# Kernel tuning notes

Measured on AMD Instinct MI355X. Metric: run time of the kernel, lower is better.

## Reference

```python
import jax, jax.numpy as jnp
import numpy as np


def _log_g(x):
    # log of g(x) = x + 0.5 for x >= 0, sigmoid(x) for x < 0 (minGRU paper, log-space)
    return jnp.where(x >= 0, jnp.log(jax.nn.relu(x) + 0.5), -jax.nn.softplus(-x))


def setup_inputs() -> dict:
    key = jax.random.key(0)
    k1, k2, k3 = jax.random.split(key, 3)
    B, L, D, H = 4, 8192, 512, 1024
    x = jax.random.normal(k1, (B, L, D), dtype=jnp.float32)
    # 1x1 conv in-projection to [hidden | gate], scaled for sane activation magnitudes
    W_in = jax.random.normal(k2, (2 * H, D), dtype=jnp.float32) * 0.05
    b_in = jnp.zeros((2 * H,), dtype=jnp.float32)
    # 1x1 conv out-projection back to model dim
    W_out = jax.random.normal(k3, (D, H), dtype=jnp.float32) * 0.05
    b_out = jnp.zeros((D,), dtype=jnp.float32)
    return {"x": x, "W_in": W_in, "b_in": b_in, "W_out": W_out, "b_out": b_out}


def reference(x, W_in, b_in, W_out, b_out):
    # x: [B, L, D]. tokenMixer transposes to [B, D, L] for MinGRU (1x1 convs),
    # which is equivalent to pointwise matmuls over the channel dim here.
    hg = jnp.einsum('bld,ed->ble', x, W_in) + b_in          # [B, L, 2H]
    H = hg.shape[-1] // 2
    hidden, gate = hg[..., :H], hg[..., H:]

    # minGRU log-space parallel scan (Heinsen associative scan):
    # h_t = (1 - z_t) * h_{t-1} + z_t * g(hidden_t), z_t = sigmoid(gate_t)
    log_coeffs = -jax.nn.softplus(gate)      # log(1 - z_t)
    log_z = -jax.nn.softplus(-gate)          # log(z_t)
    log_tilde_h = _log_g(hidden)             # log(g(hidden_t))

    a_star = jnp.cumsum(log_coeffs, axis=1)                              # [B, L, H]
    log_h = a_star + jax.lax.cumlogsumexp(log_z + log_tilde_h - a_star, axis=1)
    h = jnp.exp(log_h)                                                   # [B, L, H]

    out = jnp.einsum('blh,dh->bld', h, W_out) + b_out                    # [B, L, D]
    return out
```

## Files before the change

kernel.cpp:

```cpp
#include <hip/hip_runtime.h>
#include <hip/hip_bf16.h>
#include <cstdint>
#include <cstddef>

#define B_ 4
#define L_ 8192
#define D_ 512
#define H_ 1024
#define NC_ 256
#define LC_ (L_ / NC_)

typedef float  f32x4 __attribute__((ext_vector_type(4)));
typedef short  s16x8 __attribute__((ext_vector_type(8)));
typedef __bf16 b16x8 __attribute__((ext_vector_type(8)));

template <typename T, typename U>
__device__ inline auto mfma_sel(T a, T b, f32x4 c, U, int)
    -> decltype(__builtin_amdgcn_mfma_f32_16x16x32_bf16(a, b, c, 0, 0, 0)) {
  return __builtin_amdgcn_mfma_f32_16x16x32_bf16(a, b, c, 0, 0, 0);
}
template <typename T, typename U>
__device__ inline f32x4 mfma_sel(T a, T b, f32x4 c, U, long) {
  return __builtin_amdgcn_mfma_f32_16x16x32_bf16(
      __builtin_bit_cast(U, a), __builtin_bit_cast(U, b), c, 0, 0, 0);
}
__device__ inline f32x4 mfma_bf16_16x16x32(s16x8 a, s16x8 b, f32x4 c) {
  return mfma_sel(a, b, c, b16x8{}, 0);
}

__device__ inline ushort f2bf(float f) {
  uint32_t u = __builtin_bit_cast(uint32_t, f);
  uint32_t r = (u + 0x7fffu + ((u >> 16) & 1u)) >> 16;
  return (ushort)r;
}
__device__ inline float bf2f(ushort u) {
  return __builtin_bit_cast(float, (uint32_t)u << 16);
}

__device__ inline float softplus_f(float x) {
  return fmaxf(x, 0.f) + __logf(1.f + __expf(-fabsf(x)));
}
__device__ inline float logaddexp_f(float a, float b) {
  float m = fmaxf(a, b);
  return m + __logf(1.f + __expf(-fabsf(a - b)));
}
__device__ inline void transform_f(float hd, float g, float& lc, float& v) {
  float sp = softplus_f(g);
  lc = -sp;
  float lz = g - sp;
  float lth = (hd >= 0.f) ? __logf(hd + 0.5f) : (hd - softplus_f(hd));
  v = lz + lth;
}

__global__ void cast_kernel(const float* __restrict__ in, ushort* __restrict__ out, int n4) {
  int i = blockIdx.x * blockDim.x + threadIdx.x;
  if (i >= n4) return;
  float4 f = reinterpret_cast<const float4*>(in)[i];
  ushort4 o;
  o.x = f2bf(f.x); o.y = f2bf(f.y); o.z = f2bf(f.z); o.w = f2bf(f.w);
  reinterpret_cast<ushort4*>(out)[i] = o;
}

__global__ void cast2_kernel(const float* __restrict__ in0, ushort* __restrict__ out0, int n4_0,
                             const float* __restrict__ in1, ushort* __restrict__ out1, int n4_1) {
  int i = blockIdx.x * blockDim.x + threadIdx.x;
  const float* in; ushort* out;
  if (i < n4_0) { in = in0; out = out0; }
  else { i -= n4_0; if (i >= n4_1) return; in = in1; out = out1; }
  float4 f = reinterpret_cast<const float4*>(in)[i];
  ushort4 o;
  o.x = f2bf(f.x); o.y = f2bf(f.y); o.z = f2bf(f.z); o.w = f2bf(f.w);
  reinterpret_cast<ushort4*>(out)[i] = o;
}

#define GLDS(srcp, dstp)                                                            \
  __builtin_amdgcn_global_load_lds(                                                 \
      (const __attribute__((address_space(1))) void*)(srcp),                        \
      (__attribute__((address_space(3))) void*)(dstp), 16, 0, 0)

#define BAR()                               \
  do {                                      \
    asm volatile("" ::: "memory");          \
    __builtin_amdgcn_s_barrier();           \
    asm volatile("" ::: "memory");          \
  } while (0)

template <int MODE>
__global__ __launch_bounds__(512, 2)
void gemm_bt(const ushort* __restrict__ A, const ushort* __restrict__ Bm,
             const float* __restrict__ bias, void* __restrict__ Cv,
             int M, int N, int K) {
  __shared__ ushort As[2][256 * 64];
  __shared__ ushort Bs[2][256 * 64];
  const int tid  = threadIdx.x;
  const int wave = tid >> 6;
  const int lane = tid & 63;
  const int l15  = lane & 15;
  const int quad = lane >> 4;

  int id = blockIdx.y * gridDim.x + blockIdx.x;
  const int nwg = gridDim.x * gridDim.y;
  id = (id & 7) * (nwg >> 3) + (id >> 3);
  const int bxi = id % gridDim.x;
  const int byi = id / gridDim.x;

  const long bm = (long)byi * 256;
  const long bn = (long)bxi * 256;
  const int  wm = (wave >> 2) * 128;

  f32x4 acc[8][4];
#pragma unroll
  for (int i = 0; i < 8; ++i)
#pragma unroll
    for (int j = 0; j < 4; ++j) acc[i][j] = (f32x4){0.f, 0.f, 0.f, 0.f};

  const int rl  = lane >> 3;
  const int cb  = (lane & 7) ^ rl;
  const int srow = wave * 32 + rl;
  const ushort* gA0 = A + (bm + srow) * (long)K + cb * 8;
  const ushort* gB0;
  if (MODE == 1) {
    const long n0 = bn >> 1;
    const long grow = (srow < 128) ? (n0 + srow) : (1024 + n0 + (srow - 128));
    gB0 = Bm + grow * (long)K + cb * 8;
  } else {
    gB0 = Bm + (bn + srow) * (long)K + cb * 8;
  }
  int ldst[4];
#pragma unroll
  for (int i = 0; i < 4; ++i) ldst[i] = (wave * 32 + 8 * i) * 64;

  const int sq0 = ((0 * 4 + quad) ^ (l15 & 7)) * 8;
  const int sq1 = ((1 * 4 + quad) ^ (l15 & 7)) * 8;
  int arow[8], brow[4];
#pragma unroll
  for (int i = 0; i < 8; ++i) arow[i] = (wm + i * 16 + l15) * 64;
  if (MODE == 1) {
    const int wn0 = (wave & 3) * 32;
#pragma unroll
    for (int j = 0; j < 4; ++j) {
      const int trow = (j < 2) ? (wn0 + j * 16) : (128 + wn0 + (j - 2) * 16);
      brow[j] = (trow + l15) * 64;
    }
  } else {
    const int wn = (wave & 3) * 64;
#pragma unroll
    for (int j = 0; j < 4; ++j) brow[j] = (wn + j * 16 + l15) * 64;
  }

  const int nkt = K >> 6;

#pragma unroll
  for (int i = 0; i < 4; ++i) GLDS(gA0 + 8L * i * K, &As[0][ldst[i]]);
#pragma unroll
  for (int i = 0; i < 4; ++i) GLDS(gB0 + 8L * i * K, &Bs[0][ldst[i]]);
  asm volatile("s_waitcnt vmcnt(0)" ::: "memory");
  BAR();

  for (int t = 0; t < nkt; ++t) {
    const int buf  = t & 1;
    const int nbuf = buf ^ 1;
    const bool pf  = (t + 1) < nkt;
    const ushort* Ac = As[buf];
    const ushort* Bc = Bs[buf];
    const long koff = (long)(t + 1) * 64;
    s16x8 bf[4], af[4];

#pragma unroll
    for (int j = 0; j < 4; ++j)
      bf[j] = *reinterpret_cast<const s16x8*>(&Bc[brow[j] + sq0]);
#pragma unroll
    for (int i = 0; i < 4; ++i)
      af[i] = *reinterpret_cast<const s16x8*>(&Ac[arow[i] + sq0]);
    if (pf) {
#pragma unroll
      for (int i = 0; i < 4; ++i) GLDS(gA0 + 8L * i * K + koff, &As[nbuf][ldst[i]]);
    }
    BAR();
    __builtin_amdgcn_s_setprio(1);
#pragma unroll
    for (int i = 0; i < 4; ++i)
#pragma unroll
      for (int j = 0; j < 4; ++j)
        acc[i][j] = mfma_bf16_16x16x32(af[i], bf[j], acc[i][j]);
    __builtin_amdgcn_s_setprio(0);
    BAR();

#pragma unroll
    for (int i = 0; i < 4; ++i)
      af[i] = *reinterpret_cast<const s16x8*>(&Ac[arow[4 + i] + sq0]);
    if (pf) {
#pragma unroll
      for (int i = 0; i < 4; ++i) GLDS(gB0 + 8L * i * K + koff, &Bs[nbuf][ldst[i]]);
    }
    BAR();
    __builtin_amdgcn_s_setprio(1);
#pragma unroll
    for (int i = 0; i < 4; ++i)
#pragma unroll
      for (int j = 0; j < 4; ++j)
        acc[4 + i][j] = mfma_bf16_16x16x32(af[i], bf[j], acc[4 + i][j]);
    __builtin_amdgcn_s_setprio(0);
    BAR();

#pragma unroll
    for (int j = 0; j < 4; ++j)
      bf[j] = *reinterpret_cast<const s16x8*>(&Bc[brow[j] + sq1]);
#pragma unroll
    for (int i = 0; i < 4; ++i)
      af[i] = *reinterpret_cast<const s16x8*>(&Ac[arow[i] + sq1]);
    BAR();
    __builtin_amdgcn_s_setprio(1);
#pragma unroll
    for (int i = 0; i < 4; ++i)
#pragma unroll
      for (int j = 0; j < 4; ++j)
        acc[i][j] = mfma_bf16_16x16x32(af[i], bf[j], acc[i][j]);
    __builtin_amdgcn_s_setprio(0);
    BAR();

#pragma unroll
    for (int i = 0; i < 4; ++i)
      af[i] = *reinterpret_cast<const s16x8*>(&Ac[arow[4 + i] + sq1]);
    BAR();
    __builtin_amdgcn_s_setprio(1);
#pragma unroll
    for (int i = 0; i < 4; ++i)
#pragma unroll
      for (int j = 0; j < 4; ++j)
        acc[4 + i][j] = mfma_bf16_16x16x32(af[i], bf[j], acc[4 + i][j]);
    __builtin_amdgcn_s_setprio(0);
    if (pf) asm volatile("s_waitcnt vmcnt(0)" ::: "memory");
    BAR();
  }

  if (MODE == 1) {
    const long n0  = bn >> 1;
    const int  wn0 = (wave & 3) * 32;
#pragma unroll
    for (int mi = 0; mi < 8; ++mi) {
      const long mrow = bm + wm + mi * 16 + quad * 4;
#pragma unroll
      for (int j = 0; j < 2; ++j) {
        const long ch = n0 + wn0 + j * 16 + l15;
        const float bh = bias[ch];
        const float bg = bias[(long)(N >> 1) + ch];
        ushort* lp = (ushort*)Cv + mrow * (long)N + ch;
#pragma unroll
        for (int r = 0; r < 4; ++r) {
          float hd = acc[mi][j][r] + bh;
          float g  = acc[mi][j + 2][r] + bg;
          float lc, v; transform_f(hd, g, lc, v);
          lp[(long)r * N] = f2bf(lc);
          lp[(long)r * N + (N >> 1)] = f2bf(v);
        }
      }
    }
  } else {
    const int wn = (wave & 3) * 64;
#pragma unroll
    for (int mi = 0; mi < 8; ++mi) {
      const long mrow = bm + wm + mi * 16 + quad * 4;
#pragma unroll
      for (int ni = 0; ni < 4; ++ni) {
        const long ncol = bn + wn + ni * 16 + l15;
        const float bv = bias[ncol];
        float* cp = (float*)Cv + mrow * (long)N + ncol;
#pragma unroll
        for (int r = 0; r < 4; ++r) cp[(long)r * N] = acc[mi][ni][r] + bv;
      }
    }
  }
}

__global__ void scan_phase1(const ushort* __restrict__ hg,
                            float* __restrict__ Ac, float* __restrict__ Bc) {
  int gid = blockIdx.x * blockDim.x + threadIdx.x;
  int hq = gid & (H_ / 4 - 1);
  int c  = (gid >> 8) & (NC_ - 1);
  int b  = gid >> 16;
  const ushort* p = hg + ((size_t)(b * L_ + c * LC_) * (2 * H_)) + hq * 4;
  float As[4] = {0.f, 0.f, 0.f, 0.f};
  float Bv[4] = {-INFINITY, -INFINITY, -INFINITY, -INFINITY};
#pragma unroll 4
  for (int l = 0; l < LC_; ++l) {
    ushort4 lc4 = *reinterpret_cast<const ushort4*>(p);
    ushort4 v4  = *reinterpret_cast<const ushort4*>(p + H_);
    float lcv[4] = {bf2f(lc4.x), bf2f(lc4.y), bf2f(lc4.z), bf2f(lc4.w)};
    float vv[4]  = {bf2f(v4.x),  bf2f(v4.y),  bf2f(v4.z),  bf2f(v4.w)};
#pragma unroll
    for (int j = 0; j < 4; ++j) {
      As[j] += lcv[j];
      Bv[j] = logaddexp_f(Bv[j] + lcv[j], vv[j]);
    }
    p += 2 * H_;
  }
  size_t o = (size_t)(b * NC_ + c) * H_ + hq * 4;
  *reinterpret_cast<float4*>(&Ac[o]) = make_float4(As[0], As[1], As[2], As[3]);
  *reinterpret_cast<float4*>(&Bc[o]) = make_float4(Bv[0], Bv[1], Bv[2], Bv[3]);
}

__global__ void scan_phase2(const float* __restrict__ Ac, const float* __restrict__ Bc,
                            float* __restrict__ carry) {
  int gid = blockIdx.x * blockDim.x + threadIdx.x;
  int h = gid & (H_ - 1);
  int b = gid >> 10;
  float P = -INFINITY;
  for (int c = 0; c < NC_; ++c) {
    size_t o = (size_t)(b * NC_ + c) * H_ + h;
    carry[o] = P;
    P = logaddexp_f(P + Ac[o], Bc[o]);
  }
}

__global__ void scan_phase3(const ushort* __restrict__ hg, const float* __restrict__ carry,
                            ushort* __restrict__ hb) {
  int gid = blockIdx.x * blockDim.x + threadIdx.x;
  int hq = gid & (H_ / 4 - 1);
  int c  = (gid >> 8) & (NC_ - 1);
  int b  = gid >> 16;
  float4 cr = *reinterpret_cast<const float4*>(&carry[(size_t)(b * NC_ + c) * H_ + hq * 4]);
  float lh[4] = {cr.x, cr.y, cr.z, cr.w};
  const ushort* p = hg + ((size_t)(b * L_ + c * LC_) * (2 * H_)) + hq * 4;
  ushort* q = hb + (size_t)(b * L_ + c * LC_) * H_ + hq * 4;
#pragma unroll 4
  for (int l = 0; l < LC_; ++l) {
    ushort4 lc4 = *reinterpret_cast<const ushort4*>(p);
    ushort4 v4  = *reinterpret_cast<const ushort4*>(p + H_);
    float lcv[4] = {bf2f(lc4.x), bf2f(lc4.y), bf2f(lc4.z), bf2f(lc4.w)};
    float vv[4]  = {bf2f(v4.x),  bf2f(v4.y),  bf2f(v4.z),  bf2f(v4.w)};
    ushort4 o;
    ushort* op = &o.x;
#pragma unroll
    for (int j = 0; j < 4; ++j) {
      lh[j] = logaddexp_f(lh[j] + lcv[j], vv[j]);
      op[j] = f2bf(__expf(lh[j]));
    }
    *reinterpret_cast<ushort4*>(q) = o;
    p += 2 * H_;
    q += H_;
  }
}

extern "C" void kernel_launch(void* const* d_in, const int* in_sizes, int n_in,
                              void* d_out, int out_size, void* d_ws, size_t ws_size,
                              hipStream_t stream) {
  const float* x     = (const float*)d_in[0];
  const float* W_in  = (const float*)d_in[1];
  const float* b_in  = (const float*)d_in[2];
  const float* W_out = (const float*)d_in[3];
  const float* b_out = (const float*)d_in[4];
  float* out = (float*)d_out;

  char* ws = (char*)d_ws;
  size_t off = 0;
  auto alloc = [&](size_t bytes) {
    void* p = ws + off;
    off = (off + bytes + 255) & ~(size_t)255;
    return p;
  };
  ushort* xb    = (ushort*)alloc((size_t)B_ * L_ * H_ * 2);
  ushort* hb    = xb;
  ushort* Wib   = (ushort*)alloc((size_t)2 * H_ * D_ * 2);
  ushort* Wob   = (ushort*)alloc((size_t)D_ * H_ * 2);
  ushort* hgb   = (ushort*)alloc((size_t)B_ * L_ * 2 * H_ * 2);
  float*  Ac    = (float*)alloc((size_t)B_ * NC_ * H_ * 4);
  float*  Bc    = (float*)alloc((size_t)B_ * NC_ * H_ * 4);
  float*  carry = (float*)alloc((size_t)B_ * NC_ * H_ * 4);

  cast_kernel<<<(B_ * L_ * D_ / 4 + 255) / 256, 256, 0, stream>>>(x, xb, B_ * L_ * D_ / 4);
  {
    int n0 = 2 * H_ * D_ / 4, n1 = D_ * H_ / 4;
    cast2_kernel<<<(n0 + n1 + 255) / 256, 256, 0, stream>>>(W_in, Wib, n0, W_out, Wob, n1);
  }

  gemm_bt<1><<<dim3((2 * H_) / 256, (B_ * L_) / 256), 512, 0, stream>>>(
      xb, Wib, b_in, hgb, B_ * L_, 2 * H_, D_);

  scan_phase1<<<(B_ * NC_ * H_ / 4) / 256, 256, 0, stream>>>(hgb, Ac, Bc);
  scan_phase2<<<(B_ * H_) / 256, 256, 0, stream>>>(Ac, Bc, carry);
  scan_phase3<<<(B_ * NC_ * H_ / 4) / 256, 256, 0, stream>>>(hgb, carry, hb);

  gemm_bt<0><<<dim3(D_ / 256, (B_ * L_) / 256), 512, 0, stream>>>(
      hb, Wob, b_out, out, B_ * L_, D_, H_);
}
```

Baseline: 386.4 us.

## Halve GEMM K-tile, add BM template, use 128-row tiles for out-projection

The GEMM kernel is templated on the M tile size and its K step shrinks from 64 to 32. This halves LDS use so launch bounds can ask for 4 blocks per CU instead of 2, and the LDS swizzle and load pattern are reworked to match. The out-projection GEMM now uses 128-row tiles, which doubles its grid so the small N=512 problem fills the CUs better. The trade-off is more barrier and wait iterations per K, plus register pressure under the tighter launch bound for the 256-row variant.

```diff
diff --git a/kernel.cpp b/kernel.cpp
--- a/kernel.cpp
+++ b/kernel.cpp
@@ -85,13 +85,15 @@
     asm volatile("" ::: "memory");          \
   } while (0)
 
-template <int MODE>
-__global__ __launch_bounds__(512, 2)
+template <int MODE, int BM>
+__global__ __launch_bounds__(512, 4)
 void gemm_bt(const ushort* __restrict__ A, const ushort* __restrict__ Bm,
              const float* __restrict__ bias, void* __restrict__ Cv,
              int M, int N, int K) {
-  __shared__ ushort As[2][256 * 64];
-  __shared__ ushort Bs[2][256 * 64];
+  constexpr int MI = BM / 32;
+  constexpr int nA = BM / 128;
+  __shared__ ushort As[2][BM * 32];
+  __shared__ ushort Bs[2][256 * 32];
   const int tid  = threadIdx.x;
   const int wave = tid >> 6;
   const int lane = tid & 63;
@@ -104,141 +106,113 @@
   const int bxi = id % gridDim.x;
   const int byi = id / gridDim.x;
 
-  const long bm = (long)byi * 256;
+  const long bm = (long)byi * BM;
   const long bn = (long)bxi * 256;
-  const int  wm = (wave >> 2) * 128;
-
-  f32x4 acc[8][4];
-#pragma unroll
-  for (int i = 0; i < 8; ++i)
+  const int  wm = (wave >> 2) * (BM / 2);
+
+  f32x4 acc[MI][4];
+#pragma unroll
+  for (int i = 0; i < MI; ++i)
 #pragma unroll
     for (int j = 0; j < 4; ++j) acc[i][j] = (f32x4){0.f, 0.f, 0.f, 0.f};
 
-  const int rl  = lane >> 3;
-  const int cb  = (lane & 7) ^ rl;
-  const int srow = wave * 32 + rl;
-  const ushort* gA0 = A + (bm + srow) * (long)K + cb * 8;
+  const int rl = lane >> 2;
+  const int cb = (lane & 3) ^ ((lane >> 3) & 3);
+  const ushort* gA0 = A + (bm + wave * 16 + rl) * (long)K + cb * 8;
   const ushort* gB0;
   if (MODE == 1) {
     const long n0 = bn >> 1;
-    const long grow = (srow < 128) ? (n0 + srow) : (1024 + n0 + (srow - 128));
-    gB0 = Bm + grow * (long)K + cb * 8;
+    gB0 = Bm + (n0 + wave * 16 + rl) * (long)K + cb * 8;
   } else {
-    gB0 = Bm + (bn + srow) * (long)K + cb * 8;
-  }
-  int ldst[4];
-#pragma unroll
-  for (int i = 0; i < 4; ++i) ldst[i] = (wave * 32 + 8 * i) * 64;
-
-  const int sq0 = ((0 * 4 + quad) ^ (l15 & 7)) * 8;
-  const int sq1 = ((1 * 4 + quad) ^ (l15 & 7)) * 8;
-  int arow[8], brow[4];
-#pragma unroll
-  for (int i = 0; i < 8; ++i) arow[i] = (wm + i * 16 + l15) * 64;
+    gB0 = Bm + (bn + wave * 16 + rl) * (long)K + cb * 8;
+  }
+  const long bstep = (MODE == 1 ? 1024L : 128L) * K;
+
+  const int sq = (quad ^ ((l15 >> 1) & 3)) * 8;
+  int arow[MI], brow[4];
+#pragma unroll
+  for (int i = 0; i < MI; ++i) arow[i] = (wm + i * 16 + l15) * 32;
   if (MODE == 1) {
     const int wn0 = (wave & 3) * 32;
 #pragma unroll
     for (int j = 0; j < 4; ++j) {
       const int trow = (j < 2) ? (wn0 + j * 16) : (128 + wn0 + (j - 2) * 16);
-      brow[j] = (trow + l15) * 64;
+      brow[j] = (trow + l15) * 32;
     }
   } else {
     const int wn = (wave & 3) * 64;
 #pragma unroll
-    for (int j = 0; j < 4; ++j) brow[j] = (wn + j * 16 + l15) * 64;
-  }
-
-  const int nkt = K >> 6;
-
-#pragma unroll
-  for (int i = 0; i < 4; ++i) GLDS(gA0 + 8L * i * K, &As[0][ldst[i]]);
-#pragma unroll
-  for (int i = 0; i < 4; ++i) GLDS(gB0 + 8L * i * K, &Bs[0][ldst[i]]);
-  asm volatile("s_waitcnt vmcnt(0)" ::: "memory");
-  BAR();
+    for (int j = 0; j < 4; ++j) brow[j] = (wn + j * 16 + l15) * 32;
+  }
+
+  const int nkt = K >> 5;
+
+#pragma unroll
+  for (int i = 0; i < nA; ++i)
+    GLDS(gA0 + (128L * i) * K, &As[0][(wave * 16 + 128 * i) * 32]);
+  GLDS(gB0,         &Bs[0][(wave * 16) * 32]);
+  GLDS(gB0 + bstep, &Bs[0][(wave * 16 + 128) * 32]);
 
   for (int t = 0; t < nkt; ++t) {
+    asm volatile("s_waitcnt vmcnt(0)" ::: "memory");
+    BAR();
+
     const int buf  = t & 1;
     const int nbuf = buf ^ 1;
     const bool pf  = (t + 1) < nkt;
     const ushort* Ac = As[buf];
     const ushort* Bc = Bs[buf];
-    const long koff = (long)(t + 1) * 64;
+    const long koff = (long)(t + 1) * 32;
     s16x8 bf[4], af[4];
 
 #pragma unroll
     for (int j = 0; j < 4; ++j)
-      bf[j] = *reinterpret_cast<const s16x8*>(&Bc[brow[j] + sq0]);
-#pragma unroll
-    for (int i = 0; i < 4; ++i)
-      af[i] = *reinterpret_cast<const s16x8*>(&Ac[arow[i] + sq0]);
+      bf[j] = *reinterpret_cast<const s16x8*>(&Bc[brow[j] + sq]);
+#pragma unroll
+    for (int i = 0; i < (MI < 4 ? MI : 4); ++i)
+      af[i] = *reinterpret_cast<const s16x8*>(&Ac[arow[i] + sq]);
     if (pf) {
 #pragma unroll
-      for (int i = 0; i < 4; ++i) GLDS(gA0 + 8L * i * K + koff, &As[nbuf][ldst[i]]);
+      for (int i = 0; i < nA; ++i)
+        GLDS(gA0 + (128L * i) * K + koff, &As[nbuf][(wave * 16 + 128 * i) * 32]);
+      if (MI == 4) {
+        GLDS(gB0 + koff,         &Bs[nbuf][(wave * 16) * 32]);
+        GLDS(gB0 + bstep + koff, &Bs[nbuf][(wave * 16 + 128) * 32]);
+      }
     }
     BAR();
     __builtin_amdgcn_s_setprio(1);
 #pragma unroll
-    for (int i = 0; i < 4; ++i)
+    for (int i = 0; i < (MI < 4 ? MI : 4); ++i)
 #pragma unroll
       for (int j = 0; j < 4; ++j)
         acc[i][j] = mfma_bf16_16x16x32(af[i], bf[j], acc[i][j]);
     __builtin_amdgcn_s_setprio(0);
-    BAR();
-
-#pragma unroll
-    for (int i = 0; i < 4; ++i)
-      af[i] = *reinterpret_cast<const s16x8*>(&Ac[arow[4 + i] + sq0]);
-    if (pf) {
-#pragma unroll
-      for (int i = 0; i < 4; ++i) GLDS(gB0 + 8L * i * K + koff, &Bs[nbuf][ldst[i]]);
-    }
-    BAR();
-    __builtin_amdgcn_s_setprio(1);
-#pragma unroll
-    for (int i = 0; i < 4; ++i)
-#pragma unroll
-      for (int j = 0; j < 4; ++j)
-        acc[4 + i][j] = mfma_bf16_16x16x32(af[i], bf[j], acc[4 + i][j]);
-    __builtin_amdgcn_s_setprio(0);
-    BAR();
-
-#pragma unroll
-    for (int j = 0; j < 4; ++j)
-      bf[j] = *reinterpret_cast<const s16x8*>(&Bc[brow[j] + sq1]);
-#pragma unroll
-    for (int i = 0; i < 4; ++i)
-      af[i] = *reinterpret_cast<const s16x8*>(&Ac[arow[i] + sq1]);
-    BAR();
-    __builtin_amdgcn_s_setprio(1);
-#pragma unroll
-    for (int i = 0; i < 4; ++i)
-#pragma unroll
-      for (int j = 0; j < 4; ++j)
-        acc[i][j] = mfma_bf16_16x16x32(af[i], bf[j], acc[i][j]);
-    __builtin_amdgcn_s_setprio(0);
-    BAR();
-
-#pragma unroll
-    for (int i = 0; i < 4; ++i)
-      af[i] = *reinterpret_cast<const s16x8*>(&Ac[arow[4 + i] + sq1]);
-    BAR();
-    __builtin_amdgcn_s_setprio(1);
-#pragma unroll
-    for (int i = 0; i < 4; ++i)
-#pragma unroll
-      for (int j = 0; j < 4; ++j)
-        acc[4 + i][j] = mfma_bf16_16x16x32(af[i], bf[j], acc[4 + i][j]);
-    __builtin_amdgcn_s_setprio(0);
-    if (pf) asm volatile("s_waitcnt vmcnt(0)" ::: "memory");
-    BAR();
+
+    if (MI == 8) {
+#pragma unroll
+      for (int i = 0; i < 4; ++i)
+        af[i] = *reinterpret_cast<const s16x8*>(&Ac[arow[4 + i] + sq]);
+      if (pf) {
+        GLDS(gB0 + koff,         &Bs[nbuf][(wave * 16) * 32]);
+        GLDS(gB0 + bstep + koff, &Bs[nbuf][(wave * 16 + 128) * 32]);
+      }
+      BAR();
+      __builtin_amdgcn_s_setprio(1);
+#pragma unroll
+      for (int i = 0; i < 4; ++i)
+#pragma unroll
+        for (int j = 0; j < 4; ++j)
+          acc[4 + i][j] = mfma_bf16_16x16x32(af[i], bf[j], acc[4 + i][j]);
+      __builtin_amdgcn_s_setprio(0);
+    }
   }
 
   if (MODE == 1) {
     const long n0  = bn >> 1;
     const int  wn0 = (wave & 3) * 32;
 #pragma unroll
-    for (int mi = 0; mi < 8; ++mi) {
+    for (int mi = 0; mi < MI; ++mi) {
       const long mrow = bm + wm + mi * 16 + quad * 4;
 #pragma unroll
       for (int j = 0; j < 2; ++j) {
@@ -259,7 +233,7 @@
   } else {
     const int wn = (wave & 3) * 64;
 #pragma unroll
-    for (int mi = 0; mi < 8; ++mi) {
+    for (int mi = 0; mi < MI; ++mi) {
       const long mrow = bm + wm + mi * 16 + quad * 4;
 #pragma unroll
       for (int ni = 0; ni < 4; ++ni) {
@@ -374,13 +348,13 @@
     cast2_kernel<<<(n0 + n1 + 255) / 256, 256, 0, stream>>>(W_in, Wib, n0, W_out, Wob, n1);
   }
 
-  gemm_bt<1><<<dim3((2 * H_) / 256, (B_ * L_) / 256), 512, 0, stream>>>(
+  gemm_bt<1, 256><<<dim3((2 * H_) / 256, (B_ * L_) / 256), 512, 0, stream>>>(
       xb, Wib, b_in, hgb, B_ * L_, 2 * H_, D_);
 
   scan_phase1<<<(B_ * NC_ * H_ / 4) / 256, 256, 0, stream>>>(hgb, Ac, Bc);
   scan_phase2<<<(B_ * H_) / 256, 256, 0, stream>>>(Ac, Bc, carry);
   scan_phase3<<<(B_ * NC_ * H_ / 4) / 256, 256, 0, stream>>>(hgb, carry, hb);
 
-  gemm_bt<0><<<dim3(D_ / 256, (B_ * L_) / 256), 512, 0, stream>>>(
+  gemm_bt<0, 128><<<dim3(D_ / 256, (B_ * L_) / 128), 512, 0, stream>>>(
       hb, Wob, b_out, out, B_ * L_, D_, H_);
 }
```

New measurement: 871.0 us. 125% more time.
